# Kernel optimization log

Hardware: AMD Instinct MI355X
Metric: run time of the kernel (lower is better)

The kernel has to match this reference:

```python
import jax, jax.numpy as jnp
import numpy as np

N = 100000
E = 640000
IN, HID, OUT = 128, 256, 128


def _glorot(key, shape):
    fan_in, fan_out = shape[0], shape[1]
    lim = (6.0 / (fan_in + fan_out)) ** 0.5
    return jax.random.uniform(key, shape, jnp.float32, -lim, lim)


def setup_inputs() -> dict:
    key = jax.random.key(0)
    ks = jax.random.split(key, 8)
    x = jax.random.normal(ks[0], (N, IN), jnp.float32)
    edge_index = jax.random.randint(ks[1], (2, E), 0, N, jnp.int64)
    # conv0 MLP: in->hid->hid
    w0a = _glorot(ks[2], (IN, HID)); b0a = jnp.zeros((HID,), jnp.float32)
    w0b = _glorot(ks[3], (HID, HID)); b0b = jnp.zeros((HID,), jnp.float32)
    # conv1 MLP: hid->hid->hid
    w1a = _glorot(ks[4], (HID, HID)); b1a = jnp.zeros((HID,), jnp.float32)
    w1b = _glorot(ks[5], (HID, HID)); b1b = jnp.zeros((HID,), jnp.float32)
    # conv2 MLP: hid->out->out
    w2a = _glorot(ks[6], (HID, OUT)); b2a = jnp.zeros((OUT,), jnp.float32)
    w2b = _glorot(ks[7], (OUT, OUT)); b2b = jnp.zeros((OUT,), jnp.float32)
    return dict(x=x, edge_index=edge_index,
                w0a=w0a, b0a=b0a, w0b=w0b, b0b=b0b,
                w1a=w1a, b1a=b1a, w1b=w1b, b1b=b1b,
                w2a=w2a, b2a=b2a, w2b=w2b, b2b=b2b)


def reference(x, edge_index, w0a, b0a, w0b, b0b, w1a, b1a, w1b, b1b, w2a, b2a, w2b, b2b):
    src, dst = edge_index[0], edge_index[1]
    n = x.shape[0]
    layers = [(w0a, b0a, w0b, b0b), (w1a, b1a, w1b, b1b), (w2a, b2a, w2b, b2b)]
    for wa, ba, wb, bb in layers:
        # GINConv (eps=0): aggregate neighbor messages x[src] into dst, add self
        agg = jax.ops.segment_sum(x[src], dst, num_segments=n)  # [N, d]
        h = x + agg
        h = jnp.maximum(h @ wa + ba, 0.0) @ wb + bb  # MLP: Linear-ReLU-Linear
        x = jnp.maximum(h, 0.0)  # outer F.relu
    return x
```

## Files before the change

### kernel.cpp

```cpp
#include <hip/hip_runtime.h>
#include <hip/hip_bf16.h>

typedef __attribute__((ext_vector_type(4))) float f32x4;
typedef __attribute__((ext_vector_type(8))) short short8;
typedef unsigned short u16;

__device__ inline float bf2f(u16 u) {
    unsigned int x = ((unsigned int)u) << 16;
    return __builtin_bit_cast(float, x);
}
__device__ inline u16 f2bf(float f) {
    unsigned int x = __builtin_bit_cast(unsigned int, f);
    unsigned int r = (x + 0x7FFFu + ((x >> 16) & 1u)) >> 16;
    return (u16)r;
}

__device__ inline int edge_at(const void* edges, int flag64, long long idx) {
    if (flag64) return (int)((const long long*)edges)[idx];
    return ((const int*)edges)[idx];
}

__global__ void probe_kernel(const void* edges, int n, int* flag) {
    if (threadIdx.x == 0 && blockIdx.x == 0) {
        const long long* p = (const long long*)edges;
        int ok = 1;
        for (int i = 0; i < 64; ++i) {
            long long v = p[i];
            if (v < 0 || v >= n) { ok = 0; break; }
        }
        *flag = ok;
    }
}

__global__ void hist_kernel(const void* edges, const int* flag, int E, int* deg) {
    int f = *flag;
    for (long long i = blockIdx.x * blockDim.x + threadIdx.x; i < E;
         i += (long long)gridDim.x * blockDim.x) {
        int dst = edge_at(edges, f, (long long)E + i);
        atomicAdd(&deg[dst], 1);
    }
}

__global__ void scan1_kernel(const int* deg, int* incl, int* bsum, int n) {
    __shared__ int s[256];
    int i = blockIdx.x * 256 + threadIdx.x;
    int v = (i < n) ? deg[i] : 0;
    s[threadIdx.x] = v;
    __syncthreads();
    for (int d = 1; d < 256; d <<= 1) {
        int t = (threadIdx.x >= d) ? s[threadIdx.x - d] : 0;
        __syncthreads();
        s[threadIdx.x] += t;
        __syncthreads();
    }
    if (i < n) incl[i] = s[threadIdx.x];
    if (threadIdx.x == 255) bsum[blockIdx.x] = s[255];
}

__global__ void scan2_kernel(const int* bsum, int* boff, int nb) {
    __shared__ int s[512];
    int t = threadIdx.x;
    int v = (t < nb) ? bsum[t] : 0;
    s[t] = v;
    __syncthreads();
    for (int d = 1; d < 512; d <<= 1) {
        int u = (t >= d) ? s[t - d] : 0;
        __syncthreads();
        s[t] += u;
        __syncthreads();
    }
    boff[t] = s[t] - v;
}

__global__ void scan3_kernel(const int* incl, const int* deg, const int* boff,
                             int* offs, int* cursor, int n, int E) {
    int i = blockIdx.x * 256 + threadIdx.x;
    if (i < n) {
        int o = boff[blockIdx.x] + incl[i] - deg[i];
        offs[i] = o;
        cursor[i] = o;
    }
    if (i == 0) offs[n] = E;
}

__global__ void scatter_kernel(const void* edges, const int* flag, int E,
                               int* cursor, int* nbr) {
    int f = *flag;
    for (long long i = blockIdx.x * blockDim.x + threadIdx.x; i < E;
         i += (long long)gridDim.x * blockDim.x) {
        int src = edge_at(edges, f, i);
        int dst = edge_at(edges, f, (long long)E + i);
        int pos = atomicAdd(&cursor[dst], 1);
        nbr[pos] = src;
    }
}

__global__ void cvt_x_kernel(const float* __restrict__ x, u16* __restrict__ out, long long n4) {
    long long i = blockIdx.x * blockDim.x + threadIdx.x;
    if (i >= n4) return;
    float4 v = ((const float4*)x)[i];
    ushort4 o;
    o.x = f2bf(v.x); o.y = f2bf(v.y); o.z = f2bf(v.z); o.w = f2bf(v.w);
    ((ushort4*)out)[i] = o;
}

__global__ void cvt_w_kernel(const float* __restrict__ W, u16* __restrict__ Wt, int K, int M) {
    int i = blockIdx.x * blockDim.x + threadIdx.x;
    if (i >= K * M) return;
    int m = i / K, k = i % K;
    Wt[i] = f2bf(W[(size_t)k * M + m]);
}

template <int FP, bool BR>
__global__ __launch_bounds__(64) void agg_kernel(
    const u16* __restrict__ X, u16* __restrict__ H,
    const int* __restrict__ offs, const int* __restrict__ nbr,
    const float* __restrict__ bias, int n, int d) {
    const int node = blockIdx.x;
    const int lane = threadIdx.x;
    float acc[FP];
    const u16* xr = X + (size_t)node * d + lane * FP;
    if (FP == 2) {
        ushort2 v = *(const ushort2*)xr;
        acc[0] = bf2f(v.x); acc[1] = bf2f(v.y);
    } else {
        ushort4 v = *(const ushort4*)xr;
        acc[0] = bf2f(v.x); acc[1] = bf2f(v.y); acc[2] = bf2f(v.z); acc[3] = bf2f(v.w);
    }
    const int s = offs[node], e = offs[node + 1];
    int j = s;
    for (; j + 4 <= e; j += 4) {
        int n0 = nbr[j], n1 = nbr[j + 1], n2 = nbr[j + 2], n3 = nbr[j + 3];
        if (FP == 2) {
            ushort2 v0 = *(const ushort2*)(X + (size_t)n0 * d + lane * 2);
            ushort2 v1 = *(const ushort2*)(X + (size_t)n1 * d + lane * 2);
            ushort2 v2 = *(const ushort2*)(X + (size_t)n2 * d + lane * 2);
            ushort2 v3 = *(const ushort2*)(X + (size_t)n3 * d + lane * 2);
            acc[0] += bf2f(v0.x) + bf2f(v1.x) + bf2f(v2.x) + bf2f(v3.x);
            acc[1] += bf2f(v0.y) + bf2f(v1.y) + bf2f(v2.y) + bf2f(v3.y);
        } else {
            ushort4 v0 = *(const ushort4*)(X + (size_t)n0 * d + lane * 4);
            ushort4 v1 = *(const ushort4*)(X + (size_t)n1 * d + lane * 4);
            ushort4 v2 = *(const ushort4*)(X + (size_t)n2 * d + lane * 4);
            ushort4 v3 = *(const ushort4*)(X + (size_t)n3 * d + lane * 4);
            acc[0] += bf2f(v0.x) + bf2f(v1.x) + bf2f(v2.x) + bf2f(v3.x);
            acc[1] += bf2f(v0.y) + bf2f(v1.y) + bf2f(v2.y) + bf2f(v3.y);
            acc[2] += bf2f(v0.z) + bf2f(v1.z) + bf2f(v2.z) + bf2f(v3.z);
            acc[3] += bf2f(v0.w) + bf2f(v1.w) + bf2f(v2.w) + bf2f(v3.w);
        }
    }
    for (; j < e; ++j) {
        int nb = nbr[j];
        if (FP == 2) {
            ushort2 v = *(const ushort2*)(X + (size_t)nb * d + lane * 2);
            acc[0] += bf2f(v.x); acc[1] += bf2f(v.y);
        } else {
            ushort4 v = *(const ushort4*)(X + (size_t)nb * d + lane * 4);
            acc[0] += bf2f(v.x); acc[1] += bf2f(v.y); acc[2] += bf2f(v.z); acc[3] += bf2f(v.w);
        }
    }
    if (BR) {
#pragma unroll
        for (int q = 0; q < FP; ++q)
            acc[q] = fmaxf(acc[q] + bias[lane * FP + q], 0.f);
    }
    u16* hr = H + (size_t)node * d + lane * FP;
    if (FP == 2) {
        ushort2 o; o.x = f2bf(acc[0]); o.y = f2bf(acc[1]);
        *(ushort2*)hr = o;
    } else {
        ushort4 o; o.x = f2bf(acc[0]); o.y = f2bf(acc[1]); o.z = f2bf(acc[2]); o.w = f2bf(acc[3]);
        *(ushort4*)hr = o;
    }
}

__device__ inline f32x4 mfma16(short8 a, short8 b, f32x4 c) {
    return __builtin_amdgcn_mfma_f32_16x16x32_bf16(a, b, c, 0, 0, 0);
}

template <int K1, int M1, int M2>
__global__ __launch_bounds__(512, 2) void mlp_kernel(
    const u16* __restrict__ H, const u16* __restrict__ W1t, const float* __restrict__ b1,
    const u16* __restrict__ W2t, const float* __restrict__ b2,
    u16* __restrict__ outp, int Nrows, int ntiles) {
    constexpr int S1 = K1 + 8;
    constexpr int S2 = M1 + 16;
    constexpr int SO = M2 + 16;
    constexpr int NK1 = K1 / 32, NK2 = M1 / 32;
    constexpr int CW1 = M1 / 128, CW2 = M2 / 128;
    constexpr size_t LA = (size_t)64 * S1 * 2;
    constexpr size_t LT = (size_t)64 * S2 * 2;
    extern __shared__ char smem[];
    u16* bufA = (u16*)smem;
    u16* bufT = (u16*)(smem + LA);
    u16* bufO = (u16*)(smem + LA + LT);

    const int tid = threadIdx.x;
    const int lane = tid & 63;
    const int wid = tid >> 6;
    const int fl = lane & 15;
    const int kg = lane >> 4;
    const int rb = kg << 2;

    const int ws1 = wid * (M1 / 8);
    const int ws2 = wid * (M2 / 8);
    short8 w1f[CW1][NK1];
    short8 w2f[CW2][NK2];
    float bias1[CW1], bias2[CW2];
#pragma unroll
    for (int c = 0; c < CW1; ++c) {
        const u16* wp = W1t + (size_t)(ws1 + c * 16 + fl) * K1 + kg * 8;
        bias1[c] = b1[ws1 + c * 16 + fl];
#pragma unroll
        for (int kk = 0; kk < NK1; ++kk) w1f[c][kk] = *(const short8*)(wp + kk * 32);
    }
#pragma unroll
    for (int c = 0; c < CW2; ++c) {
        const u16* wp = W2t + (size_t)(ws2 + c * 16 + fl) * M1 + kg * 8;
        bias2[c] = b2[ws2 + c * 16 + fl];
#pragma unroll
        for (int kk = 0; kk < NK2; ++kk) w2f[c][kk] = *(const short8*)(wp + kk * 32);
    }

    constexpr int TPR = K1 / 8;
    constexpr int RPI = 512 / TPR;
    constexpr int NPASS = 64 / RPI;
    const int srow = tid / TPR;
    const int sce = (tid % TPR) * 8;

    uint4 apf[NPASS];
    auto load_tile = [&](int t) {
#pragma unroll
        for (int p = 0; p < NPASS; ++p) {
            apf[p] = make_uint4(0, 0, 0, 0);
            if (t < ntiles) {
                const int r = t * 64 + p * RPI + srow;
                if (r < Nrows) apf[p] = *(const uint4*)(H + (size_t)r * K1 + sce);
            }
        }
    };

    load_tile(blockIdx.x);

    for (int t = blockIdx.x; t < ntiles; t += gridDim.x) {
        const int r0 = t * 64;
#pragma unroll
        for (int p = 0; p < NPASS; ++p)
            *(uint4*)&bufA[(p * RPI + srow) * S1 + sce] = apf[p];
        __syncthreads();

        load_tile(t + gridDim.x);

        f32x4 acc[4][CW1];
#pragma unroll
        for (int m = 0; m < 4; ++m)
#pragma unroll
            for (int c = 0; c < CW1; ++c) acc[m][c] = (f32x4){0.f, 0.f, 0.f, 0.f};
#pragma unroll
        for (int kk = 0; kk < NK1; ++kk) {
            short8 a[4];
#pragma unroll
            for (int m = 0; m < 4; ++m)
                a[m] = *(const short8*)&bufA[(m * 16 + fl) * S1 + kk * 32 + kg * 8];
#pragma unroll
            for (int c = 0; c < CW1; ++c)
#pragma unroll
                for (int m = 0; m < 4; ++m) acc[m][c] = mfma16(a[m], w1f[c][kk], acc[m][c]);
        }

#pragma unroll
        for (int c = 0; c < CW1; ++c) {
            const int col = ws1 + c * 16 + fl;
#pragma unroll
            for (int m = 0; m < 4; ++m)
#pragma unroll
                for (int j = 0; j < 4; ++j) {
                    float v = fmaxf(acc[m][c][j] + bias1[c], 0.f);
                    bufT[(m * 16 + rb + j) * S2 + col] = f2bf(v);
                }
        }
        __syncthreads();

        f32x4 acc2[4][CW2];
#pragma unroll
        for (int m = 0; m < 4; ++m)
#pragma unroll
            for (int c = 0; c < CW2; ++c) acc2[m][c] = (f32x4){0.f, 0.f, 0.f, 0.f};
#pragma unroll
        for (int kk = 0; kk < NK2; ++kk) {
            short8 a[4];
#pragma unroll
            for (int m = 0; m < 4; ++m)
                a[m] = *(const short8*)&bufT[(m * 16 + fl) * S2 + kk * 32 + kg * 8];
#pragma unroll
            for (int c = 0; c < CW2; ++c)
#pragma unroll
                for (int m = 0; m < 4; ++m) acc2[m][c] = mfma16(a[m], w2f[c][kk], acc2[m][c]);
        }

#pragma unroll
        for (int c = 0; c < CW2; ++c) {
            const int col = ws2 + c * 16 + fl;
#pragma unroll
            for (int m = 0; m < 4; ++m)
#pragma unroll
                for (int j = 0; j < 4; ++j) {
                    float v = fmaxf(acc2[m][c][j] + bias2[c], 0.f);
                    bufO[(m * 16 + rb + j) * SO + col] = f2bf(v);
                }
        }
        __syncthreads();

        {
            constexpr int ROWB = M2 * 2;
            constexpr int TPRO = ROWB / 16;
            constexpr int RPIO = 512 / TPRO;
            const int orow = tid / TPRO;
            const int ocb = (tid % TPRO) * 16;
#pragma unroll
            for (int p = 0; p < 64 / RPIO; ++p) {
                const int row = p * RPIO + orow;
                if (r0 + row < Nrows) {
                    uint4 v = *(const uint4*)((char*)bufO + (size_t)row * SO * 2 + ocb);
                    *(uint4*)((char*)outp + (size_t)(r0 + row) * ROWB + ocb) = v;
                }
            }
        }
    }
}

template <int K, int M, bool BR, bool F32OUT>
__global__ __launch_bounds__(512, 4) void gemm1_kernel(
    const u16* __restrict__ H, const u16* __restrict__ Wt,
    const float* __restrict__ bias, void* __restrict__ outp,
    int Nrows, int ntiles) {
    constexpr int S1 = K + 8;
    constexpr int SO = F32OUT ? (M + 4) : (M + 16);
    constexpr int OB = F32OUT ? 4 : 2;
    constexpr int NK = K / 32;
    constexpr int CW = M / 128;
    constexpr size_t LA = (size_t)64 * S1 * 2;
    extern __shared__ char smem[];
    u16* bufA = (u16*)smem;
    char* bufO = smem + LA;

    const int tid = threadIdx.x;
    const int lane = tid & 63;
    const int wid = tid >> 6;
    const int fl = lane & 15;
    const int kg = lane >> 4;
    const int rb = kg << 2;

    const int ws = wid * (M / 8);
    short8 wf[CW][NK];
    float bs[CW];
#pragma unroll
    for (int c = 0; c < CW; ++c) {
        const u16* wp = Wt + (size_t)(ws + c * 16 + fl) * K + kg * 8;
        bs[c] = BR ? bias[ws + c * 16 + fl] : 0.f;
#pragma unroll
        for (int kk = 0; kk < NK; ++kk) wf[c][kk] = *(const short8*)(wp + kk * 32);
    }

    constexpr int TPR = K / 8;
    constexpr int RPI = 512 / TPR;
    constexpr int NPASS = 64 / RPI;
    const int srow = tid / TPR;
    const int sce = (tid % TPR) * 8;

    uint4 apf[NPASS];
    auto load_tile = [&](int t) {
#pragma unroll
        for (int p = 0; p < NPASS; ++p) {
            apf[p] = make_uint4(0, 0, 0, 0);
            if (t < ntiles) {
                const int r = t * 64 + p * RPI + srow;
                if (r < Nrows) apf[p] = *(const uint4*)(H + (size_t)r * K + sce);
            }
        }
    };

    load_tile(blockIdx.x);

    for (int t = blockIdx.x; t < ntiles; t += gridDim.x) {
        const int r0 = t * 64;
#pragma unroll
        for (int p = 0; p < NPASS; ++p)
            *(uint4*)&bufA[(p * RPI + srow) * S1 + sce] = apf[p];
        __syncthreads();

        load_tile(t + gridDim.x);

        f32x4 acc[4][CW];
#pragma unroll
        for (int m = 0; m < 4; ++m)
#pragma unroll
            for (int c = 0; c < CW; ++c) acc[m][c] = (f32x4){0.f, 0.f, 0.f, 0.f};
#pragma unroll
        for (int kk = 0; kk < NK; ++kk) {
            short8 a[4];
#pragma unroll
            for (int m = 0; m < 4; ++m)
                a[m] = *(const short8*)&bufA[(m * 16 + fl) * S1 + kk * 32 + kg * 8];
#pragma unroll
            for (int c = 0; c < CW; ++c)
#pragma unroll
                for (int m = 0; m < 4; ++m) acc[m][c] = mfma16(a[m], wf[c][kk], acc[m][c]);
        }

#pragma unroll
        for (int c = 0; c < CW; ++c) {
            const int col = ws + c * 16 + fl;
#pragma unroll
            for (int m = 0; m < 4; ++m)
#pragma unroll
                for (int j = 0; j < 4; ++j) {
                    float v = acc[m][c][j];
                    if (BR) v = fmaxf(v + bs[c], 0.f);
                    const int row = m * 16 + rb + j;
                    if (F32OUT)
                        ((float*)bufO)[row * SO + col] = v;
                    else
                        ((u16*)bufO)[row * SO + col] = f2bf(v);
                }
        }
        __syncthreads();

        {
            constexpr int ROWB = M * OB;
            constexpr int TPRO = ROWB / 16;
            constexpr int RPIO = 512 / TPRO;
            const int orow = tid / TPRO;
            const int ocb = (tid % TPRO) * 16;
#pragma unroll
            for (int p = 0; p < 64 / RPIO; ++p) {
                const int row = p * RPIO + orow;
                if (r0 + row < Nrows) {
                    uint4 v = *(const uint4*)(bufO + (size_t)row * SO * OB + ocb);
                    *(uint4*)((char*)outp + (size_t)(r0 + row) * ROWB + ocb) = v;
                }
            }
        }
    }
}

extern "C" void kernel_launch(void* const* d_in, const int* in_sizes, int n_in,
                              void* d_out, int out_size, void* d_ws, size_t ws_size,
                              hipStream_t stream) {
    const int IN = 128, HID = 256, OUTD = 128;
    const int N = in_sizes[0] / IN;
    const int E = in_sizes[1] / 2;

    const float* x = (const float*)d_in[0];
    const void* edges = d_in[1];
    const float* w0a = (const float*)d_in[2];  const float* b0a = (const float*)d_in[3];
    const float* w0b = (const float*)d_in[4];  const float* b0b = (const float*)d_in[5];
    const float* w1a = (const float*)d_in[6];  const float* b1a = (const float*)d_in[7];
    const float* w1b = (const float*)d_in[8];  const float* b1b = (const float*)d_in[9];
    const float* w2a = (const float*)d_in[10]; const float* b2a = (const float*)d_in[11];
    const float* w2b = (const float*)d_in[12]; const float* b2b = (const float*)d_in[13];

    char* ws = (char*)d_ws;
    size_t off = 0;
    auto alloc = [&](size_t b) { size_t o = off; off = (off + b + 255) & ~(size_t)255; return o; };
    int* flag   = (int*)(ws + alloc(4));
    int* deg    = (int*)(ws + alloc((size_t)N * 4));
    int* incl   = (int*)(ws + alloc((size_t)N * 4));
    int* bsum   = (int*)(ws + alloc(512 * 4));
    int* boff   = (int*)(ws + alloc(512 * 4));
    int* offs   = (int*)(ws + alloc((size_t)(N + 1) * 4));
    int* cursor = (int*)(ws + alloc((size_t)N * 4));
    int* nbr    = (int*)(ws + alloc((size_t)E * 4));
    u16* wt0a = (u16*)(ws + alloc((size_t)IN * HID * 2));
    u16* wt0b = (u16*)(ws + alloc((size_t)HID * HID * 2));
    u16* wt1a = (u16*)(ws + alloc((size_t)HID * HID * 2));
    u16* wt1b = (u16*)(ws + alloc((size_t)HID * HID * 2));
    u16* wt2a = (u16*)(ws + alloc((size_t)HID * OUTD * 2));
    u16* wt2b = (u16*)(ws + alloc((size_t)OUTD * OUTD * 2));
    u16* Pa = (u16*)(ws + alloc((size_t)N * HID * 2));
    u16* Pb = (u16*)(ws + alloc((size_t)N * HID * 2));

    probe_kernel<<<1, 64, 0, stream>>>(edges, N, flag);
    hipMemsetAsync(deg, 0, (size_t)N * 4, stream);
    hist_kernel<<<2048, 256, 0, stream>>>(edges, flag, E, deg);
    int nb1 = (N + 255) / 256;
    scan1_kernel<<<nb1, 256, 0, stream>>>(deg, incl, bsum, N);
    scan2_kernel<<<1, 512, 0, stream>>>(bsum, boff, nb1);
    scan3_kernel<<<nb1, 256, 0, stream>>>(incl, deg, boff, offs, cursor, N, E);
    scatter_kernel<<<2048, 256, 0, stream>>>(edges, flag, E, cursor, nbr);

    long long n4 = (long long)N * IN / 4;
    cvt_x_kernel<<<(int)((n4 + 255) / 256), 256, 0, stream>>>(x, Pa, n4);
    cvt_w_kernel<<<(IN * HID + 255) / 256, 256, 0, stream>>>(w0a, wt0a, IN, HID);
    cvt_w_kernel<<<(HID * HID + 255) / 256, 256, 0, stream>>>(w0b, wt0b, HID, HID);
    cvt_w_kernel<<<(HID * HID + 255) / 256, 256, 0, stream>>>(w1a, wt1a, HID, HID);
    cvt_w_kernel<<<(HID * HID + 255) / 256, 256, 0, stream>>>(w1b, wt1b, HID, HID);
    cvt_w_kernel<<<(HID * OUTD + 255) / 256, 256, 0, stream>>>(w2a, wt2a, HID, OUTD);
    cvt_w_kernel<<<(OUTD * OUTD + 255) / 256, 256, 0, stream>>>(w2b, wt2b, OUTD, OUTD);

    const int ntiles = (N + 63) / 64;
    const int pgrid = ntiles < 256 ? ntiles : 256;
    const int ggrid = ntiles < 512 ? ntiles : 512;

    const size_t mlp_lds0 = (size_t)64 * (128 + 8) * 2 + (size_t)64 * (256 + 16) * 2 * 2;
    const size_t mlp_lds1 = (size_t)64 * (256 + 8) * 2 + (size_t)64 * (256 + 16) * 2 * 2;
    const size_t pre_lds  = (size_t)64 * (256 + 8) * 2 + (size_t)64 * (128 + 16) * 2;
    const size_t fin_lds  = (size_t)64 * (128 + 8) * 2 + (size_t)64 * (128 + 4) * 4;

    agg_kernel<2, false><<<N, 64, 0, stream>>>(Pa, Pb, offs, nbr, nullptr, N, IN);
    mlp_kernel<128, 256, 256><<<pgrid, 512, mlp_lds0, stream>>>(Pb, wt0a, b0a, wt0b, b0b, Pa, N, ntiles);
    agg_kernel<4, false><<<N, 64, 0, stream>>>(Pa, Pb, offs, nbr, nullptr, N, HID);
    mlp_kernel<256, 256, 256><<<pgrid, 512, mlp_lds1, stream>>>(Pb, wt1a, b1a, wt1b, b1b, Pa, N, ntiles);
    gemm1_kernel<256, 128, false, false><<<ggrid, 512, pre_lds, stream>>>(Pa, wt2a, nullptr, Pb, N, ntiles);
    agg_kernel<2, true><<<N, 64, 0, stream>>>(Pb, Pa, offs, nbr, b2a, N, OUTD);
    gemm1_kernel<128, 128, true, true><<<ggrid, 512, fin_lds, stream>>>(Pa, wt2b, b2b, d_out, N, ntiles);
}
```

Measured before the change: 341.4 us.

## Batch multiple nodes per aggregation block with wider loads and fuse weight conversions

The aggregation kernel now packs 4–8 nodes per 256-thread block: one wavefront per node for 256-wide features, and half-wavefronts for 128-wide features, with every lane doing 8-byte loads. It prefetches up to 8 neighbour indices and rows up front so more loads are in flight, then walks the remaining neighbours in chunks of 4 under a wave-uniform loop. The six weight-conversion launches are merged into a single kernel driven by a prefix-offset table. The goal is to cut block-launch overhead and raise memory-level parallelism in the gather, at the cost of more registers and predicated loads.

```diff
diff --git a/kernel.cpp b/kernel.cpp
--- a/kernel.cpp
+++ b/kernel.cpp
@@ -104,74 +104,89 @@
     ((ushort4*)out)[i] = o;
 }
 
-__global__ void cvt_w_kernel(const float* __restrict__ W, u16* __restrict__ Wt, int K, int M) {
+struct WcvtArgs {
+    const float* w[6];
+    u16* o[6];
+    int K[6], M[6];
+    int pre[7];
+};
+__global__ void cvt_w_all_kernel(WcvtArgs a) {
     int i = blockIdx.x * blockDim.x + threadIdx.x;
-    if (i >= K * M) return;
-    int m = i / K, k = i % K;
-    Wt[i] = f2bf(W[(size_t)k * M + m]);
-}
-
-template <int FP, bool BR>
-__global__ __launch_bounds__(64) void agg_kernel(
+    if (i >= a.pre[6]) return;
+    int mi = 0;
+#pragma unroll
+    for (int q = 1; q < 6; ++q) mi += (i >= a.pre[q]);
+    int loc = i - a.pre[mi];
+    int K = a.K[mi], M = a.M[mi];
+    int m = loc / K, k = loc % K;
+    a.o[mi][loc] = f2bf(a.w[mi][(size_t)k * M + m]);
+}
+
+template <int NPW, bool BR>
+__global__ __launch_bounds__(256) void agg_kernel(
     const u16* __restrict__ X, u16* __restrict__ H,
     const int* __restrict__ offs, const int* __restrict__ nbr,
-    const float* __restrict__ bias, int n, int d) {
-    const int node = blockIdx.x;
-    const int lane = threadIdx.x;
-    float acc[FP];
-    const u16* xr = X + (size_t)node * d + lane * FP;
-    if (FP == 2) {
-        ushort2 v = *(const ushort2*)xr;
-        acc[0] = bf2f(v.x); acc[1] = bf2f(v.y);
-    } else {
-        ushort4 v = *(const ushort4*)xr;
-        acc[0] = bf2f(v.x); acc[1] = bf2f(v.y); acc[2] = bf2f(v.z); acc[3] = bf2f(v.w);
-    }
+    const float* __restrict__ bias, int n) {
+    constexpr int D = (NPW == 1) ? 256 : 128;
+    const int tid = threadIdx.x;
+    const int wid = tid >> 6;
+    const int lane = tid & 63;
+    const int sub = (NPW == 2) ? (lane >> 5) : 0;
+    const int sl = (NPW == 2) ? (lane & 31) : lane;
+    const int node = blockIdx.x * (4 * NPW) + wid * NPW + sub;
+    if (node >= n) return;
+
     const int s = offs[node], e = offs[node + 1];
-    int j = s;
-    for (; j + 4 <= e; j += 4) {
-        int n0 = nbr[j], n1 = nbr[j + 1], n2 = nbr[j + 2], n3 = nbr[j + 3];
-        if (FP == 2) {
-            ushort2 v0 = *(const ushort2*)(X + (size_t)n0 * d + lane * 2);
-            ushort2 v1 = *(const ushort2*)(X + (size_t)n1 * d + lane * 2);
-            ushort2 v2 = *(const ushort2*)(X + (size_t)n2 * d + lane * 2);
-            ushort2 v3 = *(const ushort2*)(X + (size_t)n3 * d + lane * 2);
-            acc[0] += bf2f(v0.x) + bf2f(v1.x) + bf2f(v2.x) + bf2f(v3.x);
-            acc[1] += bf2f(v0.y) + bf2f(v1.y) + bf2f(v2.y) + bf2f(v3.y);
-        } else {
-            ushort4 v0 = *(const ushort4*)(X + (size_t)n0 * d + lane * 4);
-            ushort4 v1 = *(const ushort4*)(X + (size_t)n1 * d + lane * 4);
-            ushort4 v2 = *(const ushort4*)(X + (size_t)n2 * d + lane * 4);
-            ushort4 v3 = *(const ushort4*)(X + (size_t)n3 * d + lane * 4);
-            acc[0] += bf2f(v0.x) + bf2f(v1.x) + bf2f(v2.x) + bf2f(v3.x);
-            acc[1] += bf2f(v0.y) + bf2f(v1.y) + bf2f(v2.y) + bf2f(v3.y);
-            acc[2] += bf2f(v0.z) + bf2f(v1.z) + bf2f(v2.z) + bf2f(v3.z);
-            acc[3] += bf2f(v0.w) + bf2f(v1.w) + bf2f(v2.w) + bf2f(v3.w);
-        }
-    }
-    for (; j < e; ++j) {
-        int nb = nbr[j];
-        if (FP == 2) {
-            ushort2 v = *(const ushort2*)(X + (size_t)nb * d + lane * 2);
-            acc[0] += bf2f(v.x); acc[1] += bf2f(v.y);
-        } else {
-            ushort4 v = *(const ushort4*)(X + (size_t)nb * d + lane * 4);
-            acc[0] += bf2f(v.x); acc[1] += bf2f(v.y); acc[2] += bf2f(v.z); acc[3] += bf2f(v.w);
-        }
-    }
+    const int cnt = min(e - s, 8);
+
+    ushort4 sv = *(const ushort4*)(X + (size_t)node * D + sl * 4);
+    int idx[8];
+#pragma unroll
+    for (int q = 0; q < 8; ++q)
+        if (q < cnt) idx[q] = nbr[s + q];
+    ushort4 rv[8];
+#pragma unroll
+    for (int q = 0; q < 8; ++q)
+        if (q < cnt) rv[q] = *(const ushort4*)(X + (size_t)idx[q] * D + sl * 4);
+
+    float acc[4] = {bf2f(sv.x), bf2f(sv.y), bf2f(sv.z), bf2f(sv.w)};
+#pragma unroll
+    for (int q = 0; q < 8; ++q)
+        if (q < cnt) {
+            acc[0] += bf2f(rv[q].x); acc[1] += bf2f(rv[q].y);
+            acc[2] += bf2f(rv[q].z); acc[3] += bf2f(rv[q].w);
+        }
+
+    int j = s + 8;
+    while (__any(j < e)) {
+        const int c2 = e - j;
+        ushort4 tv[4];
+        int ti[4];
+#pragma unroll
+        for (int q = 0; q < 4; ++q)
+            if (q < c2) ti[q] = nbr[j + q];
+#pragma unroll
+        for (int q = 0; q < 4; ++q)
+            if (q < c2) tv[q] = *(const ushort4*)(X + (size_t)ti[q] * D + sl * 4);
+#pragma unroll
+        for (int q = 0; q < 4; ++q)
+            if (q < c2) {
+                acc[0] += bf2f(tv[q].x); acc[1] += bf2f(tv[q].y);
+                acc[2] += bf2f(tv[q].z); acc[3] += bf2f(tv[q].w);
+            }
+        j += 4;
+    }
+
     if (BR) {
-#pragma unroll
-        for (int q = 0; q < FP; ++q)
-            acc[q] = fmaxf(acc[q] + bias[lane * FP + q], 0.f);
-    }
-    u16* hr = H + (size_t)node * d + lane * FP;
-    if (FP == 2) {
-        ushort2 o; o.x = f2bf(acc[0]); o.y = f2bf(acc[1]);
-        *(ushort2*)hr = o;
-    } else {
-        ushort4 o; o.x = f2bf(acc[0]); o.y = f2bf(acc[1]); o.z = f2bf(acc[2]); o.w = f2bf(acc[3]);
-        *(ushort4*)hr = o;
-    }
+        float4 b4 = *(const float4*)&bias[sl * 4];
+        acc[0] = fmaxf(acc[0] + b4.x, 0.f);
+        acc[1] = fmaxf(acc[1] + b4.y, 0.f);
+        acc[2] = fmaxf(acc[2] + b4.z, 0.f);
+        acc[3] = fmaxf(acc[3] + b4.w, 0.f);
+    }
+    ushort4 o;
+    o.x = f2bf(acc[0]); o.y = f2bf(acc[1]); o.z = f2bf(acc[2]); o.w = f2bf(acc[3]);
+    *(ushort4*)(H + (size_t)node * D + sl * 4) = o;
 }
 
 __device__ inline f32x4 mfma16(short8 a, short8 b, f32x4 c) {
@@ -491,12 +506,18 @@
 
     long long n4 = (long long)N * IN / 4;
     cvt_x_kernel<<<(int)((n4 + 255) / 256), 256, 0, stream>>>(x, Pa, n4);
-    cvt_w_kernel<<<(IN * HID + 255) / 256, 256, 0, stream>>>(w0a, wt0a, IN, HID);
-    cvt_w_kernel<<<(HID * HID + 255) / 256, 256, 0, stream>>>(w0b, wt0b, HID, HID);
-    cvt_w_kernel<<<(HID * HID + 255) / 256, 256, 0, stream>>>(w1a, wt1a, HID, HID);
-    cvt_w_kernel<<<(HID * HID + 255) / 256, 256, 0, stream>>>(w1b, wt1b, HID, HID);
-    cvt_w_kernel<<<(HID * OUTD + 255) / 256, 256, 0, stream>>>(w2a, wt2a, HID, OUTD);
-    cvt_w_kernel<<<(OUTD * OUTD + 255) / 256, 256, 0, stream>>>(w2b, wt2b, OUTD, OUTD);
+    {
+        WcvtArgs a;
+        a.w[0] = w0a; a.o[0] = wt0a; a.K[0] = IN;   a.M[0] = HID;
+        a.w[1] = w0b; a.o[1] = wt0b; a.K[1] = HID;  a.M[1] = HID;
+        a.w[2] = w1a; a.o[2] = wt1a; a.K[2] = HID;  a.M[2] = HID;
+        a.w[3] = w1b; a.o[3] = wt1b; a.K[3] = HID;  a.M[3] = HID;
+        a.w[4] = w2a; a.o[4] = wt2a; a.K[4] = HID;  a.M[4] = OUTD;
+        a.w[5] = w2b; a.o[5] = wt2b; a.K[5] = OUTD; a.M[5] = OUTD;
+        a.pre[0] = 0;
+        for (int q = 0; q < 6; ++q) a.pre[q + 1] = a.pre[q] + a.K[q] * a.M[q];
+        cvt_w_all_kernel<<<(a.pre[6] + 255) / 256, 256, 0, stream>>>(a);
+    }
 
     const int ntiles = (N + 63) / 64;
     const int pgrid = ntiles < 256 ? ntiles : 256;
@@ -507,11 +528,11 @@
     const size_t pre_lds  = (size_t)64 * (256 + 8) * 2 + (size_t)64 * (128 + 16) * 2;
     const size_t fin_lds  = (size_t)64 * (128 + 8) * 2 + (size_t)64 * (128 + 4) * 4;
 
-    agg_kernel<2, false><<<N, 64, 0, stream>>>(Pa, Pb, offs, nbr, nullptr, N, IN);
+    agg_kernel<2, false><<<(N + 7) / 8, 256, 0, stream>>>(Pa, Pb, offs, nbr, nullptr, N);
     mlp_kernel<128, 256, 256><<<pgrid, 512, mlp_lds0, stream>>>(Pb, wt0a, b0a, wt0b, b0b, Pa, N, ntiles);
-    agg_kernel<4, false><<<N, 64, 0, stream>>>(Pa, Pb, offs, nbr, nullptr, N, HID);
+    agg_kernel<1, false><<<(N + 3) / 4, 256, 0, stream>>>(Pa, Pb, offs, nbr, nullptr, N);
     mlp_kernel<256, 256, 256><<<pgrid, 512, mlp_lds1, stream>>>(Pb, wt1a, b1a, wt1b, b1b, Pa, N, ntiles);
     gemm1_kernel<256, 128, false, false><<<ggrid, 512, pre_lds, stream>>>(Pa, wt2a, nullptr, Pb, N, ntiles);
-    agg_kernel<2, true><<<N, 64, 0, stream>>>(Pb, Pa, offs, nbr, b2a, N, OUTD);
+    agg_kernel<2, true><<<(N + 7) / 8, 256, 0, stream>>>(Pb, Pa, offs, nbr, b2a, N);
     gemm1_kernel<128, 128, true, true><<<ggrid, 512, fin_lds, stream>>>(Pa, wt2b, b2b, d_out, N, ntiles);
 }
```

Measured after the change: 349.4 us. 2.3% more time.
